# Kernel optimization log

Measured on AMD Instinct MI355X. Metric: run time of the kernel, lower is better.

## Reference

```python
import jax, jax.numpy as jnp
import numpy as np

K = 3        # kernel size
PAD = 1      # padding
DG = 16      # deformable groups
MAXR = 10.0  # max_residue_magnitude


def _lrelu(x):
    return jnp.where(x >= 0, x, 0.1 * x)


def _conv3(x, w, b):
    y = jax.lax.conv_general_dilated(x, w, (1, 1), 'SAME',
                                     dimension_numbers=('NCHW', 'OIHW', 'NCHW'))
    return y + b[None, :, None, None]


def _deform_conv2d(x, offset, mask, weight, bias):
    # x: [B,Cin,H,W]; offset: [B,2*DG*K*K,H,W]; mask: [B,DG*K*K,H,W]
    B, Cin, H, W = x.shape
    Cout = weight.shape[0]
    G, Cg, K2 = DG, Cin // DG, K * K
    off = offset.reshape(B, G, K2, 2, H, W)
    dy, dx = off[:, :, :, 0], off[:, :, :, 1]
    ky = jnp.repeat(jnp.arange(K), K).astype(x.dtype)   # [K2]
    kx = jnp.tile(jnp.arange(K), K).astype(x.dtype)
    hh = jnp.arange(H, dtype=x.dtype)
    ww = jnp.arange(W, dtype=x.dtype)
    # sampling positions [B,G,K2,H,W]
    py = dy + ky[None, None, :, None, None] + hh[None, None, None, :, None] - PAD
    px = dx + kx[None, None, :, None, None] + ww[None, None, None, None, :] - PAD
    y0 = jnp.floor(py)
    x0 = jnp.floor(px)
    wy1 = py - y0
    wx1 = px - x0
    xf = x.reshape(B, G, Cg, H * W)

    def gather(yi, xi, wgt):
        valid = (yi >= 0) & (yi <= H - 1) & (xi >= 0) & (xi <= W - 1)
        idx = (jnp.clip(yi, 0, H - 1).astype(jnp.int32) * W
               + jnp.clip(xi, 0, W - 1).astype(jnp.int32)).reshape(B, G, -1)
        vals = jnp.take_along_axis(
            xf, jnp.broadcast_to(idx[:, :, None, :], (B, G, Cg, idx.shape[-1])), axis=3)
        vals = vals.reshape(B, G, Cg, K2, H, W)
        w = (wgt * valid.astype(x.dtype))[:, :, None]  # [B,G,1,K2,H,W]
        return vals * w

    s = (gather(y0, x0, (1 - wy1) * (1 - wx1))
         + gather(y0, x0 + 1, (1 - wy1) * wx1)
         + gather(y0 + 1, x0, wy1 * (1 - wx1))
         + gather(y0 + 1, x0 + 1, wy1 * wx1))
    s = s * mask.reshape(B, G, K2, H, W)[:, :, None]
    wr = weight.reshape(Cout, G, Cg, K2)
    out = jnp.einsum('ogck,bgckhw->bohw', wr, s)
    return out + bias[None, :, None, None]


def setup_inputs() -> dict:
    key = jax.random.key(0)
    ks = jax.random.split(key, 16)
    B, Cin, Cout, H, W = 4, 128, 64, 96, 96
    Coff = 3 * Cout + 4  # 196
    stdv = 1.0 / np.sqrt(Cin * K * K)
    inp = {
        'x': jax.random.normal(ks[0], (B, Cin, H, W), jnp.float32),
        'extra_feat': jax.random.normal(ks[1], (B, 3 * Cout, H, W), jnp.float32),
        'flow_1': jax.random.normal(ks[2], (B, 2, H, W), jnp.float32),
        'flow_2': jax.random.normal(ks[3], (B, 2, H, W), jnp.float32),
        'weight': jax.random.uniform(ks[4], (Cout, Cin, K, K), jnp.float32, -stdv, stdv),
        'bias': jax.random.normal(ks[5], (Cout,), jnp.float32) * 0.01,
        'ow0': jax.random.normal(ks[6], (Cout, Coff, K, K), jnp.float32) * 0.02,
        'ob0': jnp.zeros((Cout,), jnp.float32),
        'ow1': jax.random.normal(ks[7], (Cout, Cout, K, K), jnp.float32) * 0.02,
        'ob1': jnp.zeros((Cout,), jnp.float32),
        'ow2': jax.random.normal(ks[8], (Cout, Cout, K, K), jnp.float32) * 0.02,
        'ob2': jnp.zeros((Cout,), jnp.float32),
        'ow3': jax.random.normal(ks[9], (27 * DG, Cout, K, K), jnp.float32) * 0.01,
        'ob3': jnp.zeros((27 * DG,), jnp.float32),
    }
    return inp


def reference(x, extra_feat, flow_1, flow_2, weight, bias,
              ow0, ob0, ow1, ob1, ow2, ob2, ow3, ob3):
    feat = jnp.concatenate([extra_feat, flow_1, flow_2], axis=1)
    h = _lrelu(_conv3(feat, ow0, ob0))
    h = _lrelu(_conv3(h, ow1, ob1))
    h = _lrelu(_conv3(h, ow2, ob2))
    out = _conv3(h, ow3, ob3)
    o1, o2, m = jnp.split(out, 3, axis=1)
    offs = MAXR * jnp.tanh(jnp.concatenate([o1, o2], axis=1))
    off1, off2 = jnp.split(offs, 2, axis=1)
    off1 = off1 + jnp.tile(flow_1[:, ::-1], (1, off1.shape[1] // 2, 1, 1))
    off2 = off2 + jnp.tile(flow_2[:, ::-1], (1, off2.shape[1] // 2, 1, 1))
    offset = jnp.concatenate([off1, off2], axis=1)
    mask = jax.nn.sigmoid(m)
    return _deform_conv2d(x, offset, mask, weight, bias)
```

## Files before the change

kernel.cpp:

```cpp
#include <hip/hip_runtime.h>
#include <math.h>

#define HW 9216
#define Hh 96
#define Ww 96
#define PHW 9604

typedef __attribute__((ext_vector_type(8))) short bh8;
typedef __attribute__((ext_vector_type(4))) short bh4;
typedef __attribute__((ext_vector_type(4))) float f32x4;
typedef __attribute__((ext_vector_type(2))) float f32x2;

__device__ __forceinline__ short f2bf(float f) {
    union { float f; unsigned u; } v; v.f = f;
    unsigned r = v.u + 0x7FFFu + ((v.u >> 16) & 1u);
    return (short)(r >> 16);
}
__device__ __forceinline__ float bf2f(short s) {
    union { unsigned u; float f; } v; v.u = ((unsigned)(unsigned short)s) << 16;
    return v.f;
}

__global__ void zero_borders(short* __restrict__ xpad1,
                             short* __restrict__ hpa,
                             short* __restrict__ hpb) {
    int i = blockIdx.x * 256 + threadIdx.x;
    const int n1 = 4 * 388 * 224, n2 = 4 * 388 * 64;
    short* p; int C;
    if (i < n1) { p = xpad1; C = 224; }
    else if (i < n1 + n2) { p = hpa; C = 64; i -= n1; }
    else if (i < n1 + 2 * n2) { p = hpb; C = 64; i -= n1 + n2; }
    else return;
    int c = i % C;
    int r = i / C;
    int b = r / 388, pid = r - b * 388;
    int row, col;
    if (pid < 98)       { row = 0;  col = pid; }
    else if (pid < 196) { row = 97; col = pid - 98; }
    else if (pid < 292) { row = pid - 196 + 1; col = 0; }
    else                { row = pid - 292 + 1; col = 97; }
    p[((size_t)b * PHW + row * 98 + col) * C + c] = 0;
}

__global__ void pack_x1(const float* __restrict__ extra,
                        const float* __restrict__ f1,
                        const float* __restrict__ f2,
                        short* __restrict__ xp) {
    __shared__ float t[32][33];
    const int tid = threadIdx.x, tx = tid & 31, ty = tid >> 5;
    const int pt = blockIdx.x, ct = blockIdx.y, b = blockIdx.z;
#pragma unroll
    for (int j = 0; j < 4; ++j) {
        int ch = ct * 32 + ty + j * 8;
        int p = pt * 32 + tx;
        float v = 0.f;
        if (ch < 192)      v = extra[(b * 192 + ch) * HW + p];
        else if (ch < 194) v = f1[(b * 2 + ch - 192) * HW + p];
        else if (ch < 196) v = f2[(b * 2 + ch - 194) * HW + p];
        t[ty + j * 8][tx] = v;
    }
    __syncthreads();
#pragma unroll
    for (int j = 0; j < 4; ++j) {
        int pr = ty + j * 8;
        int p = pt * 32 + pr;
        int r = p / 96, c = p - r * 96;
        xp[((size_t)b * PHW + (r + 1) * 98 + (c + 1)) * 224 + ct * 32 + tx] =
            f2bf(t[tx][pr]);
    }
}

__global__ void pack_xd(const float* __restrict__ x, short* __restrict__ xd) {
    __shared__ float t[32][33];
    const int tid = threadIdx.x, tx = tid & 31, ty = tid >> 5;
    const int pt = blockIdx.x, ct = blockIdx.y, b = blockIdx.z;
#pragma unroll
    for (int j = 0; j < 4; ++j) {
        int ch = ct * 32 + ty + j * 8;
        t[ty + j * 8][tx] = x[((size_t)b * 128 + ch) * HW + pt * 32 + tx];
    }
    __syncthreads();
    if (tid < 128) {
        int oct = tid >> 5, p = tid & 31;
        int g = (ct * 32 + oct * 8) >> 3;
        bh8 v;
#pragma unroll
        for (int c = 0; c < 8; ++c) v[c] = f2bf(t[oct * 8 + c][p]);
        *(bh8*)&xd[(((size_t)b * 16 + g) * HW + pt * 32 + p) * 8] = v;
    }
}

__global__ void prep_weights(const float* __restrict__ ow0, const float* __restrict__ ow1,
                             const float* __restrict__ ow2, const float* __restrict__ ow3,
                             const float* __restrict__ wd,
                             short* __restrict__ wb0, short* __restrict__ wb1,
                             short* __restrict__ wb2, short* __restrict__ wb3,
                             short* __restrict__ wbd) {
    int i = blockIdx.x * 256 + threadIdx.x;
    const int n0 = 64 * 9 * 224, n1 = 64 * 9 * 64, n3 = 448 * 9 * 64, nd = 64 * 1152;
    if (i < n0) {
        int co = i / (9 * 224); int r = i - co * (9 * 224);
        int tap = r / 224, ci = r - tap * 224;
        wb0[i] = f2bf(ci < 196 ? ow0[(co * 196 + ci) * 9 + tap] : 0.f);
        return;
    }
    i -= n0;
    if (i < n1) {
        int co = i / (9 * 64); int r = i - co * (9 * 64);
        int tap = r / 64, ci = r - tap * 64;
        wb1[i] = f2bf(ow1[(co * 64 + ci) * 9 + tap]);
        return;
    }
    i -= n1;
    if (i < n1) {
        int co = i / (9 * 64); int r = i - co * (9 * 64);
        int tap = r / 64, ci = r - tap * 64;
        wb2[i] = f2bf(ow2[(co * 64 + ci) * 9 + tap]);
        return;
    }
    i -= n1;
    if (i < n3) {
        int co = i / (9 * 64); int r = i - co * (9 * 64);
        int tap = r / 64, ci = r - tap * 64;
        wb3[i] = f2bf(co < 432 ? ow3[(co * 64 + ci) * 9 + tap] : 0.f);
        return;
    }
    i -= n3;
    if (i < nd) {
        int co = i / 1152, kd = i - co * 1152;
        int gt = kd >> 3, c = kd & 7;
        int g = gt / 9, tap = gt - g * 9;
        wbd[i] = f2bf(wd[(co * 128 + g * 8 + c) * 9 + tap]);
    }
}

template<int CINP, int KCH, int PIX>
__launch_bounds__(256)
__global__ void conv_mfma(const short* __restrict__ xp,
                          const short* __restrict__ wb,
                          const float* __restrict__ bias,
                          short* __restrict__ o1) {
    __shared__ __attribute__((aligned(16))) short smA[9 * 64 * 32];
    const int tid = threadIdx.x;
    const int lane = tid & 63, wv = tid >> 6;
    const int q = lane >> 4, l15 = lane & 15;
    const int b = blockIdx.y;
    const int pix0 = blockIdx.x * (64 * PIX) + wv * (16 * PIX);

    int soh[PIX], sow[PIX];
    const short* bp[PIX];
#pragma unroll
    for (int s = 0; s < PIX; ++s) {
        int pixs = pix0 + s * 16;
        soh[s] = pixs / 96;
        sow[s] = pixs - soh[s] * 96;
        bp[s] = xp + ((size_t)b * PHW + soh[s] * 98 + sow[s] + l15) * CINP + q * 8;
    }

    const int sco = tid >> 2, sqq = tid & 3;
    const short* wsrc = wb + (size_t)sco * (9 * CINP) + sqq * 8;

    f32x4 acc[PIX][4];
#pragma unroll
    for (int s = 0; s < PIX; ++s)
#pragma unroll
        for (int t = 0; t < 4; ++t) acc[s][t] = (f32x4){0.f, 0.f, 0.f, 0.f};

    for (int p = 0; p < KCH; ++p) {
        __syncthreads();
        bh8 wtmp[9];
#pragma unroll
        for (int tap = 0; tap < 9; ++tap)
            wtmp[tap] = *(const bh8*)(wsrc + tap * CINP + p * 32);
#pragma unroll
        for (int tap = 0; tap < 9; ++tap)
            *(bh8*)&smA[tap * 2048 + sco * 32 + sqq * 8] = wtmp[tap];
        __syncthreads();
#pragma unroll
        for (int tap = 0; tap < 9; ++tap) {
            const int ky = tap / 3, kx = tap - (tap / 3) * 3;
            bh8 bf[PIX];
#pragma unroll
            for (int s = 0; s < PIX; ++s)
                bf[s] = *(const bh8*)(bp[s] + (ky * 98 + kx) * CINP + p * 32);
#pragma unroll
            for (int t = 0; t < 4; ++t) {
                bh8 af = *(const bh8*)&smA[tap * 2048 + (t * 16 + l15) * 32 + q * 8];
#pragma unroll
                for (int s = 0; s < PIX; ++s)
                    acc[s][t] = __builtin_amdgcn_mfma_f32_16x16x32_bf16(
                        af, bf[s], acc[s][t], 0, 0, 0);
            }
        }
    }

#pragma unroll
    for (int s = 0; s < PIX; ++s) {
        size_t base = ((size_t)b * PHW + (soh[s] + 1) * 98 + sow[s] + l15 + 1) * 64;
#pragma unroll
        for (int t = 0; t < 4; ++t) {
            bh4 v4;
#pragma unroll
            for (int r = 0; r < 4; ++r) {
                int co = t * 16 + q * 4 + r;
                float v = acc[s][t][r] + bias[co];
                v = (v >= 0.f) ? v : 0.1f * v;
                v4[r] = f2bf(v);
            }
            *(bh4*)(o1 + base + t * 16 + q * 4) = v4;
        }
    }
}

__launch_bounds__(256)
__global__ void conv4_gemm(const short* __restrict__ xp,
                           const short* __restrict__ wb,
                           const float* __restrict__ bias,
                           float* __restrict__ offp,
                           short* __restrict__ maskb,
                           const float* __restrict__ flow1,
                           const float* __restrict__ flow2) {
    __shared__ __attribute__((aligned(16))) short smA[64 * 40];
    __shared__ __attribute__((aligned(16))) short smB[192 * 40];
    const int tid = threadIdx.x;
    const int lane = tid & 63, wv = tid >> 6;
    const int q = lane >> 4, l15 = lane & 15;
    const int pg = blockIdx.x;
    const int b = blockIdx.y;
    const int cob = blockIdx.z * 64;
    const int r0 = pg * 2;

    const int a_co = tid >> 2, a_ks = tid & 3;
    const short* asrc = wb + (size_t)(cob + a_co) * 576 + a_ks * 8;

    f32x4 acc[3][4];
#pragma unroll
    for (int pf = 0; pf < 3; ++pf)
#pragma unroll
        for (int cf = 0; cf < 4; ++cf) acc[pf][cf] = (f32x4){0.f, 0.f, 0.f, 0.f};

    for (int ch = 0; ch < 18; ++ch) {
        const int tap = ch >> 1, ci = (ch & 1) * 32;
        const int ky = tap / 3, kx = tap - (tap / 3) * 3;
        __syncthreads();
        *(bh8*)&smA[a_co * 40 + a_ks * 8] = *(const bh8*)(asrc + tap * 64 + ci);
#pragma unroll
        for (int it = 0; it < 3; ++it) {
            int id = it * 256 + tid;
            int sp = id >> 2, ks = id & 3;
            int srow = (sp >= 96) ? 1 : 0;
            int scol = sp - srow * 96;
            *(bh8*)&smB[sp * 40 + ks * 8] = *(const bh8*)&xp[
                ((size_t)b * PHW + (r0 + srow + ky) * 98 + scol + kx) * 64 + ci + ks * 8];
        }
        __syncthreads();
        bh8 bf[3], af[4];
#pragma unroll
        for (int pf = 0; pf < 3; ++pf)
            bf[pf] = *(const bh8*)&smB[(wv * 48 + pf * 16 + l15) * 40 + q * 8];
#pragma unroll
        for (int cf = 0; cf < 4; ++cf)
            af[cf] = *(const bh8*)&smA[(cf * 16 + l15) * 40 + q * 8];
#pragma unroll
        for (int pf = 0; pf < 3; ++pf)
#pragma unroll
            for (int cf = 0; cf < 4; ++cf)
                acc[pf][cf] = __builtin_amdgcn_mfma_f32_16x16x32_bf16(
                    af[cf], bf[pf], acc[pf][cf], 0, 0, 0);
    }

#pragma unroll
    for (int pf = 0; pf < 3; ++pf) {
        int local = wv * 48 + pf * 16 + l15;
        int lrow = (local >= 96) ? 1 : 0;
        int pix = (r0 + lrow) * 96 + (local - lrow * 96);
#pragma unroll
        for (int cf = 0; cf < 4; ++cf) {
#pragma unroll
            for (int r = 0; r < 4; ++r) {
                int chn = cob + cf * 16 + q * 4 + r;
                if (chn < 432) {
                    float v = acc[pf][cf][r] + bias[chn];
                    if (chn < 288) {
                        float tt = 10.f * tanhf(v);
                        const float* fl = (chn < 144) ? flow1 : flow2;
                        float fv = fl[(b * 2 + (1 - (chn & 1))) * HW + pix];
                        offp[(((size_t)b * 144 + (chn >> 1)) * HW + pix) * 2 + (chn & 1)] = tt + fv;
                    } else {
                        maskb[((size_t)b * 144 + (chn - 288)) * HW + pix] =
                            f2bf(1.f / (1.f + expf(-v)));
                    }
                }
            }
        }
    }
}

__global__ void deform_mfma(const short* __restrict__ xd,
                            const float* __restrict__ offp,
                            const short* __restrict__ maskb,
                            const short* __restrict__ wbd,
                            const float* __restrict__ bias,
                            float* __restrict__ out) {
    __shared__ float red[4][1024];
    const int tid = threadIdx.x;
    const int lane = tid & 63, wv = tid >> 6;
    const int q = lane >> 4, l15 = lane & 15;
    const int blk = blockIdx.x;
    const int xs = blk & 7, idx = blk >> 3;
    const int b = xs >> 1;
    const int pix0 = ((xs & 1) * 288 + idx) * 16;
    const int pix = pix0 + l15;
    const int h = pix / 96, w = pix - (pix / 96) * 96;

    const float* opp = offp + ((size_t)b * 144 * HW + pix) * 2;
    const short* mp = maskb + (size_t)b * 144 * HW + pix;
    const short* xb = xd + (size_t)b * 16 * HW * 8;
    const short* ap = wbd + (size_t)l15 * 1152 + wv * 288 + q * 8;

    f32x2 dxy[9];
    float mk[9];
#pragma unroll
    for (int i = 0; i < 9; ++i) {
        const int gt = wv * 36 + i * 4 + q;
        dxy[i] = *(const f32x2*)(opp + (size_t)gt * HW * 2);
        mk[i] = bf2f(mp[(size_t)gt * HW]);
    }

    f32x4 acc[4];
#pragma unroll
    for (int t = 0; t < 4; ++t) acc[t] = (f32x4){0.f, 0.f, 0.f, 0.f};

#pragma unroll
    for (int i = 0; i < 9; ++i) {
        const int gt = wv * 36 + i * 4 + q;
        const int g = gt / 9, tap = gt - (gt / 9) * 9;
        float py = dxy[i][0] + (float)(tap / 3) + (float)h - 1.f;
        float px = dxy[i][1] + (float)(tap - (tap / 3) * 3) + (float)w - 1.f;
        float y0f = floorf(py), x0f = floorf(px);
        float wy1 = py - y0f, wx1 = px - x0f;
        float wy0 = 1.f - wy1, wx0 = 1.f - wx1;
        int y0 = (int)y0f, x0 = (int)x0f;
        int y1 = y0 + 1, x1 = x0 + 1;
        bool vy0 = (y0 >= 0) && (y0 < Hh), vy1 = (y1 >= 0) && (y1 < Hh);
        bool vx0 = (x0 >= 0) && (x0 < Ww), vx1 = (x1 >= 0) && (x1 < Ww);
        int cy0 = min(max(y0, 0), Hh - 1), cy1 = min(max(y1, 0), Hh - 1);
        int cx0 = min(max(x0, 0), Ww - 1), cx1 = min(max(x1, 0), Ww - 1);
        float m = mk[i];
        float w00 = wy0 * wx0 * ((vy0 && vx0) ? m : 0.f);
        float w01 = wy0 * wx1 * ((vy0 && vx1) ? m : 0.f);
        float w10 = wy1 * wx0 * ((vy1 && vx0) ? m : 0.f);
        float w11 = wy1 * wx1 * ((vy1 && vx1) ? m : 0.f);
        const short* cb = xb + (size_t)g * HW * 8;
        bh8 a00 = *(const bh8*)(cb + (size_t)(cy0 * 96 + cx0) * 8);
        bh8 a01 = *(const bh8*)(cb + (size_t)(cy0 * 96 + cx1) * 8);
        bh8 a10 = *(const bh8*)(cb + (size_t)(cy1 * 96 + cx0) * 8);
        bh8 a11 = *(const bh8*)(cb + (size_t)(cy1 * 96 + cx1) * 8);
        bh8 bf;
#pragma unroll
        for (int c = 0; c < 8; ++c) {
            float s = w00 * bf2f(a00[c]) + w01 * bf2f(a01[c])
                    + w10 * bf2f(a10[c]) + w11 * bf2f(a11[c]);
            bf[c] = f2bf(s);
        }
#pragma unroll
        for (int t = 0; t < 4; ++t) {
            bh8 af = *(const bh8*)(ap + (size_t)t * 16 * 1152 + i * 32);
            acc[t] = __builtin_amdgcn_mfma_f32_16x16x32_bf16(af, bf, acc[t], 0, 0, 0);
        }
    }

#pragma unroll
    for (int t = 0; t < 4; ++t)
#pragma unroll
        for (int r = 0; r < 4; ++r)
            red[wv][(t * 16 + q * 4 + r) * 16 + l15] = acc[t][r];
    __syncthreads();
    for (int e = tid; e < 1024; e += 256) {
        int co = e >> 4, pl = e & 15;
        float v = red[0][e] + red[1][e] + red[2][e] + red[3][e] + bias[co];
        out[((size_t)b * 64 + co) * HW + pix0 + pl] = v;
    }
}

extern "C" void kernel_launch(void* const* d_in, const int* in_sizes, int n_in,
                              void* d_out, int out_size, void* d_ws, size_t ws_size,
                              hipStream_t stream) {
    const float* x      = (const float*)d_in[0];
    const float* extra  = (const float*)d_in[1];
    const float* flow1  = (const float*)d_in[2];
    const float* flow2  = (const float*)d_in[3];
    const float* weight = (const float*)d_in[4];
    const float* bias   = (const float*)d_in[5];
    const float* ow0    = (const float*)d_in[6];
    const float* ob0    = (const float*)d_in[7];
    const float* ow1    = (const float*)d_in[8];
    const float* ob1    = (const float*)d_in[9];
    const float* ow2    = (const float*)d_in[10];
    const float* ob2    = (const float*)d_in[11];
    const float* ow3    = (const float*)d_in[12];
    const float* ob3    = (const float*)d_in[13];
    float* out = (float*)d_out;

    char* wsb = (char*)d_ws;
    short* xpad1 = (short*)wsb;   wsb += (size_t)4 * PHW * 224 * 2;
    short* hpa   = (short*)wsb;   wsb += (size_t)4 * PHW * 64 * 2;
    short* hpb   = (short*)wsb;   wsb += (size_t)4 * PHW * 64 * 2;
    float* offpair = (float*)wsb; wsb += (size_t)4 * 144 * HW * 2 * 4;
    short* maskbuf = (short*)wsb; wsb += (size_t)4 * 144 * HW * 2;
    short* xd      = (short*)wsb; wsb += (size_t)4 * 16 * HW * 8 * 2 + 32;
    short* wb0     = (short*)wsb; wsb += 64 * 9 * 224 * 2;
    short* wb1     = (short*)wsb; wsb += 64 * 9 * 64 * 2;
    short* wb2     = (short*)wsb; wsb += 64 * 9 * 64 * 2;
    short* wb3     = (short*)wsb; wsb += 448 * 9 * 64 * 2;
    short* wbd     = (short*)wsb;

    auto g1 = [](int n) { return dim3((n + 255) / 256); };
    zero_borders<<<g1(4 * 388 * 352), 256, 0, stream>>>(xpad1, hpa, hpb);
    pack_x1<<<dim3(288, 7, 4), 256, 0, stream>>>(extra, flow1, flow2, xpad1);
    pack_xd<<<dim3(288, 4, 4), 256, 0, stream>>>(x, xd);
    prep_weights<<<g1(534528), 256, 0, stream>>>(ow0, ow1, ow2, ow3, weight,
                                                 wb0, wb1, wb2, wb3, wbd);

    conv_mfma<224, 7, 1><<<dim3(144, 4), 256, 0, stream>>>(xpad1, wb0, ob0, hpa);
    conv_mfma<64, 2, 1><<<dim3(144, 4), 256, 0, stream>>>(hpa, wb1, ob1, hpb);
    conv_mfma<64, 2, 1><<<dim3(144, 4), 256, 0, stream>>>(hpb, wb2, ob2, hpa);
    conv4_gemm<<<dim3(48, 4, 7), 256, 0, stream>>>(hpa, wb3, ob3, offpair,
                                                   maskbuf, flow1, flow2);
    deform_mfma<<<dim3(2304), 256, 0, stream>>>(xd, offpair, maskbuf, wbd, bias, out);
}
```

Measured before the change: 314.8 us.

## Split conv output channels across waves, full-tap LDS staging with XOR swizzle in conv4

```diff
diff --git a/kernel.cpp b/kernel.cpp
--- a/kernel.cpp
+++ b/kernel.cpp
@@ -134,7 +134,7 @@
     }
 }
 
-template<int CINP, int KCH, int PIX>
+template<int CINP, int KCH>
 __launch_bounds__(256)
 __global__ void conv_mfma(const short* __restrict__ xp,
                           const short* __restrict__ wb,
@@ -145,26 +145,18 @@
     const int lane = tid & 63, wv = tid >> 6;
     const int q = lane >> 4, l15 = lane & 15;
     const int b = blockIdx.y;
-    const int pix0 = blockIdx.x * (64 * PIX) + wv * (16 * PIX);
-
-    int soh[PIX], sow[PIX];
-    const short* bp[PIX];
-#pragma unroll
-    for (int s = 0; s < PIX; ++s) {
-        int pixs = pix0 + s * 16;
-        soh[s] = pixs / 96;
-        sow[s] = pixs - soh[s] * 96;
-        bp[s] = xp + ((size_t)b * PHW + soh[s] * 98 + sow[s] + l15) * CINP + q * 8;
-    }
+    const int strip = wv >> 1, coh = wv & 1;
+    const int pix0 = blockIdx.x * 32 + strip * 16;
+    const int soh = pix0 / 96, sow = pix0 - (pix0 / 96) * 96;
+
+    const short* bp = xp + ((size_t)b * PHW + soh * 98 + sow + l15) * CINP + q * 8;
 
     const int sco = tid >> 2, sqq = tid & 3;
     const short* wsrc = wb + (size_t)sco * (9 * CINP) + sqq * 8;
 
-    f32x4 acc[PIX][4];
-#pragma unroll
-    for (int s = 0; s < PIX; ++s)
-#pragma unroll
-        for (int t = 0; t < 4; ++t) acc[s][t] = (f32x4){0.f, 0.f, 0.f, 0.f};
+    f32x4 acc[2];
+#pragma unroll
+    for (int t = 0; t < 2; ++t) acc[t] = (f32x4){0.f, 0.f, 0.f, 0.f};
 
     for (int p = 0; p < KCH; ++p) {
         __syncthreads();
@@ -179,36 +171,27 @@
 #pragma unroll
         for (int tap = 0; tap < 9; ++tap) {
             const int ky = tap / 3, kx = tap - (tap / 3) * 3;
-            bh8 bf[PIX];
-#pragma unroll
-            for (int s = 0; s < PIX; ++s)
-                bf[s] = *(const bh8*)(bp[s] + (ky * 98 + kx) * CINP + p * 32);
-#pragma unroll
-            for (int t = 0; t < 4; ++t) {
-                bh8 af = *(const bh8*)&smA[tap * 2048 + (t * 16 + l15) * 32 + q * 8];
-#pragma unroll
-                for (int s = 0; s < PIX; ++s)
-                    acc[s][t] = __builtin_amdgcn_mfma_f32_16x16x32_bf16(
-                        af, bf[s], acc[s][t], 0, 0, 0);
+            bh8 bf = *(const bh8*)(bp + (ky * 98 + kx) * CINP + p * 32);
+#pragma unroll
+            for (int t = 0; t < 2; ++t) {
+                bh8 af = *(const bh8*)&smA[tap * 2048 + ((coh * 2 + t) * 16 + l15) * 32 + q * 8];
+                acc[t] = __builtin_amdgcn_mfma_f32_16x16x32_bf16(af, bf, acc[t], 0, 0, 0);
             }
         }
     }
 
-#pragma unroll
-    for (int s = 0; s < PIX; ++s) {
-        size_t base = ((size_t)b * PHW + (soh[s] + 1) * 98 + sow[s] + l15 + 1) * 64;
-#pragma unroll
-        for (int t = 0; t < 4; ++t) {
-            bh4 v4;
-#pragma unroll
-            for (int r = 0; r < 4; ++r) {
-                int co = t * 16 + q * 4 + r;
-                float v = acc[s][t][r] + bias[co];
-                v = (v >= 0.f) ? v : 0.1f * v;
-                v4[r] = f2bf(v);
-            }
-            *(bh4*)(o1 + base + t * 16 + q * 4) = v4;
-        }
+    size_t base = ((size_t)b * PHW + (soh + 1) * 98 + sow + l15 + 1) * 64;
+#pragma unroll
+    for (int t = 0; t < 2; ++t) {
+        bh4 v4;
+#pragma unroll
+        for (int r = 0; r < 4; ++r) {
+            int co = coh * 32 + t * 16 + q * 4 + r;
+            float v = acc[t][r] + bias[co];
+            v = (v >= 0.f) ? v : 0.1f * v;
+            v4[r] = f2bf(v);
+        }
+        *(bh4*)(o1 + base + coh * 32 + t * 16 + q * 4) = v4;
     }
 }
 
@@ -220,8 +203,8 @@
                            short* __restrict__ maskb,
                            const float* __restrict__ flow1,
                            const float* __restrict__ flow2) {
-    __shared__ __attribute__((aligned(16))) short smA[64 * 40];
-    __shared__ __attribute__((aligned(16))) short smB[192 * 40];
+    __shared__ __attribute__((aligned(16))) short smA[64 * 64];
+    __shared__ __attribute__((aligned(16))) short smB[192 * 64];
     const int tid = threadIdx.x;
     const int lane = tid & 63, wv = tid >> 6;
     const int q = lane >> 4, l15 = lane & 15;
@@ -230,43 +213,56 @@
     const int cob = blockIdx.z * 64;
     const int r0 = pg * 2;
 
-    const int a_co = tid >> 2, a_ks = tid & 3;
-    const short* asrc = wb + (size_t)(cob + a_co) * 576 + a_ks * 8;
-
     f32x4 acc[3][4];
 #pragma unroll
     for (int pf = 0; pf < 3; ++pf)
 #pragma unroll
         for (int cf = 0; cf < 4; ++cf) acc[pf][cf] = (f32x4){0.f, 0.f, 0.f, 0.f};
 
-    for (int ch = 0; ch < 18; ++ch) {
-        const int tap = ch >> 1, ci = (ch & 1) * 32;
+    for (int tap = 0; tap < 9; ++tap) {
         const int ky = tap / 3, kx = tap - (tap / 3) * 3;
         __syncthreads();
-        *(bh8*)&smA[a_co * 40 + a_ks * 8] = *(const bh8*)(asrc + tap * 64 + ci);
-#pragma unroll
-        for (int it = 0; it < 3; ++it) {
+#pragma unroll
+        for (int it = 0; it < 2; ++it) {
             int id = it * 256 + tid;
-            int sp = id >> 2, ks = id & 3;
-            int srow = (sp >= 96) ? 1 : 0;
-            int scol = sp - srow * 96;
-            *(bh8*)&smB[sp * 40 + ks * 8] = *(const bh8*)&xp[
-                ((size_t)b * PHW + (r0 + srow + ky) * 98 + scol + kx) * 64 + ci + ks * 8];
+            int row = id >> 3, s = id & 7;
+            int sw = s ^ (row & 7);
+            *(bh8*)&smA[row * 64 + sw * 8] =
+                *(const bh8*)(wb + (size_t)(cob + row) * 576 + tap * 64 + s * 8);
+        }
+#pragma unroll
+        for (int it = 0; it < 6; ++it) {
+            int id = it * 256 + tid;
+            int row = id >> 3, s = id & 7;
+            int sw = s ^ (row & 7);
+            int srow = (row >= 96) ? 1 : 0;
+            int scol = row - srow * 96;
+            *(bh8*)&smB[row * 64 + sw * 8] = *(const bh8*)&xp[
+                ((size_t)b * PHW + (r0 + srow + ky) * 98 + scol + kx) * 64 + s * 8];
         }
         __syncthreads();
-        bh8 bf[3], af[4];
-#pragma unroll
-        for (int pf = 0; pf < 3; ++pf)
-            bf[pf] = *(const bh8*)&smB[(wv * 48 + pf * 16 + l15) * 40 + q * 8];
-#pragma unroll
-        for (int cf = 0; cf < 4; ++cf)
-            af[cf] = *(const bh8*)&smA[(cf * 16 + l15) * 40 + q * 8];
-#pragma unroll
-        for (int pf = 0; pf < 3; ++pf)
-#pragma unroll
-            for (int cf = 0; cf < 4; ++cf)
-                acc[pf][cf] = __builtin_amdgcn_mfma_f32_16x16x32_bf16(
-                    af[cf], bf[pf], acc[pf][cf], 0, 0, 0);
+#pragma unroll
+        for (int kc = 0; kc < 2; ++kc) {
+            bh8 bf[3], af[4];
+#pragma unroll
+            for (int pf = 0; pf < 3; ++pf) {
+                int row = wv * 48 + pf * 16 + l15;
+                int sw = (kc * 4 + q) ^ (row & 7);
+                bf[pf] = *(const bh8*)&smB[row * 64 + sw * 8];
+            }
+#pragma unroll
+            for (int cf = 0; cf < 4; ++cf) {
+                int row = cf * 16 + l15;
+                int sw = (kc * 4 + q) ^ (row & 7);
+                af[cf] = *(const bh8*)&smA[row * 64 + sw * 8];
+            }
+#pragma unroll
+            for (int pf = 0; pf < 3; ++pf)
+#pragma unroll
+                for (int cf = 0; cf < 4; ++cf)
+                    acc[pf][cf] = __builtin_amdgcn_mfma_f32_16x16x32_bf16(
+                        af[cf], bf[pf], acc[pf][cf], 0, 0, 0);
+        }
     }
 
 #pragma unroll
@@ -276,17 +272,24 @@
         int pix = (r0 + lrow) * 96 + (local - lrow * 96);
 #pragma unroll
         for (int cf = 0; cf < 4; ++cf) {
-#pragma unroll
-            for (int r = 0; r < 4; ++r) {
-                int chn = cob + cf * 16 + q * 4 + r;
-                if (chn < 432) {
-                    float v = acc[pf][cf][r] + bias[chn];
-                    if (chn < 288) {
-                        float tt = 10.f * tanhf(v);
-                        const float* fl = (chn < 144) ? flow1 : flow2;
-                        float fv = fl[(b * 2 + (1 - (chn & 1))) * HW + pix];
-                        offp[(((size_t)b * 144 + (chn >> 1)) * HW + pix) * 2 + (chn & 1)] = tt + fv;
-                    } else {
+            int cb0 = cob + cf * 16 + q * 4;
+            if (cb0 < 288) {
+                const float* fl = (cb0 < 144) ? flow1 : flow2;
+                float fe = fl[(b * 2 + 1) * HW + pix];
+                float fo = fl[(b * 2) * HW + pix];
+                float t0 = 10.f * tanhf(acc[pf][cf][0] + bias[cb0 + 0]) + fe;
+                float t1 = 10.f * tanhf(acc[pf][cf][1] + bias[cb0 + 1]) + fo;
+                float t2 = 10.f * tanhf(acc[pf][cf][2] + bias[cb0 + 2]) + fe;
+                float t3 = 10.f * tanhf(acc[pf][cf][3] + bias[cb0 + 3]) + fo;
+                size_t p0 = ((size_t)b * 144 + (cb0 >> 1)) * HW + pix;
+                *(f32x2*)&offp[p0 * 2] = (f32x2){t0, t1};
+                *(f32x2*)&offp[(p0 + HW) * 2] = (f32x2){t2, t3};
+            } else {
+#pragma unroll
+                for (int r = 0; r < 4; ++r) {
+                    int chn = cb0 + r;
+                    if (chn < 432) {
+                        float v = acc[pf][cf][r] + bias[chn];
                         maskb[((size_t)b * 144 + (chn - 288)) * HW + pix] =
                             f2bf(1.f / (1.f + expf(-v)));
                     }
@@ -422,9 +425,9 @@
     prep_weights<<<g1(534528), 256, 0, stream>>>(ow0, ow1, ow2, ow3, weight,
                                                  wb0, wb1, wb2, wb3, wbd);
 
-    conv_mfma<224, 7, 1><<<dim3(144, 4), 256, 0, stream>>>(xpad1, wb0, ob0, hpa);
-    conv_mfma<64, 2, 1><<<dim3(144, 4), 256, 0, stream>>>(hpa, wb1, ob1, hpb);
-    conv_mfma<64, 2, 1><<<dim3(144, 4), 256, 0, stream>>>(hpb, wb2, ob2, hpa);
+    conv_mfma<224, 7><<<dim3(288, 4), 256, 0, stream>>>(xpad1, wb0, ob0, hpa);
+    conv_mfma<64, 2><<<dim3(288, 4), 256, 0, stream>>>(hpa, wb1, ob1, hpb);
+    conv_mfma<64, 2><<<dim3(288, 4), 256, 0, stream>>>(hpb, wb2, ob2, hpa);
     conv4_gemm<<<dim3(48, 4, 7), 256, 0, stream>>>(hpa, wb3, ob3, offpair,
                                                    maskbuf, flow1, flow2);
     deform_mfma<<<dim3(2304), 256, 0, stream>>>(xd, offpair, maskbuf, wbd, bias, out);
```

Result: slower. 333.5 us (+5.9%).
